# Kernel tuning notes

Hardware: AMD Instinct MI355X
Metric: run time of the kernel (lower is better)

## Reference

```python
import jax, jax.numpy as jnp
import numpy as np

TOP_K = 2000
NUM_DETS = 1000
BASE_LAYER_RANGE = (24.0, 48.0, 24.0, 48.0)  # (min_y, max_y, min_x, max_x) from db.configs


def _topk(heat, K):
    # heat: [B, C, H, W] -> topk over flattened C*H*W (CornerNet-style)
    B, C, H, W = heat.shape
    scores, inds = jax.lax.top_k(heat.reshape(B, -1), K)
    clses = inds // (H * W)
    sp_inds = inds % (H * W)            # spatial index into H*W
    ys = (sp_inds // W).astype(heat.dtype)
    xs = (sp_inds % W).astype(heat.dtype)
    return scores, sp_inds, clses, ys, xs


def _transpose_and_gather(feat, ind):
    # feat: [B, C, H, W], ind: [B, K] spatial indices -> [B, K, C]
    B, C, H, W = feat.shape
    feat = feat.transpose(0, 2, 3, 1).reshape(B, H * W, C)
    return feat[jnp.arange(B)[:, None], ind]


def _gather_feat(feat, ind):
    # feat: [B, N, C], ind: [B, K] -> [B, K, C]
    B = feat.shape[0]
    return feat[jnp.arange(B)[:, None], ind]


def _decode_layer(heat, tl_regr, br_regr, H0, W0, layer_idx):
    B, C, H, W = heat.shape
    dt = heat.dtype
    height_scale = 8.0 * H0 / H
    width_scale = 8.0 * W0 / W
    K = min(TOP_K, H * W)
    scores, inds, clses, ys, xs = _topk(heat, K)
    ys = ys.reshape(B, K, 1)
    xs = xs.reshape(B, K, 1)
    tlr = _transpose_and_gather(tl_regr, inds).reshape(B, K, 1, 2)
    brr = _transpose_and_gather(br_regr, inds).reshape(B, K, 1, 2)
    min_y, max_y, min_x, max_x = [v / 8.0 / 2.0 for v in BASE_LAYER_RANGE]
    tl_xs = xs - ((max_x - min_x) * tlr[..., 0] + (max_x + min_x) / 2.0)
    tl_ys = ys - ((max_y - min_y) * tlr[..., 1] + (max_y + min_y) / 2.0)
    br_xs = xs + ((max_x - min_x) * brr[..., 0] + (max_x + min_x) / 2.0)
    br_ys = ys + ((max_y - min_y) * brr[..., 1] + (max_y + min_y) / 2.0)
    bboxes = jnp.stack((tl_xs, tl_ys, br_xs, br_ys), axis=3)  # [B, K, 1, 4]
    sc = scores.reshape(B, K, 1)
    invalid = (br_xs < tl_xs) | (br_ys < tl_ys)
    sc = jnp.where(invalid, jnp.asarray(-1.0, dt), sc)
    sc = sc.reshape(B, -1)
    nd = min(NUM_DETS, sc.shape[1])
    sc, top = jax.lax.top_k(sc, nd)
    sc = sc[:, :, None]
    bboxes = _gather_feat(bboxes.reshape(B, -1, 4), top)
    bboxes = bboxes * jnp.asarray([width_scale, height_scale, width_scale, height_scale], dt)
    # layer_detections: zeros [B, nd, 7]; [:,:,:5] = cat([scores, bboxes]); then row 6 set to i
    det = jnp.concatenate([sc, bboxes, jnp.zeros((B, nd, 2), dt)], axis=2)
    det = det.at[:, 6, :].set(jnp.asarray(float(layer_idx), dt))  # faithful to `[:, 6] = i`
    return det


def setup_inputs() -> dict:
    key = jax.random.key(0)
    ks = jax.random.split(key, 9)
    B, C = 16, 80
    sizes = [(128, 128), (64, 64), (32, 32)]
    inp = {}
    for i, (H, W) in enumerate(sizes):
        inp[f"heat{i}"] = jax.random.uniform(ks[3 * i], (B, C, H, W), dtype=jnp.float32)
        inp[f"tl{i}"] = jax.random.normal(ks[3 * i + 1], (B, 2, H, W), dtype=jnp.float32)
        inp[f"br{i}"] = jax.random.normal(ks[3 * i + 2], (B, 2, H, W), dtype=jnp.float32)
    return inp


def reference(heat0, heat1, heat2, tl0, tl1, tl2, br0, br1, br2):
    heats = [heat0, heat1, heat2]
    tls = [tl0, tl1, tl2]
    brs = [br0, br1, br2]
    _, _, H0, W0 = heats[0].shape
    dets = [_decode_layer(heats[i], tls[i], brs[i], H0, W0, i) for i in range(3)]
    detections = jnp.concatenate(dets, axis=1)  # [B, sum_nd, 7]
    nd = min(NUM_DETS, detections.shape[1])
    _, top = jax.lax.top_k(detections[:, :, 0], nd)
    return _gather_feat(detections, top)
```

## Files before the change

### kernel.cpp

```cpp
#include <hip/hip_runtime.h>


#define NB 1024
#define CHUNK 32768

__device__ __forceinline__ unsigned int ord_f32(float f) {
    unsigned int b = __float_as_uint(f);
    return (b & 0x80000000u) ? ~b : (b | 0x80000000u);
}
__device__ __forceinline__ float unord_f32(unsigned int o) {
    unsigned int b = (o & 0x80000000u) ? (o & 0x7fffffffu) : ~o;
    return __uint_as_float(b);
}
__device__ __forceinline__ int bucket_of(float f) {
    int bi = (int)(f * (float)NB);
    bi = bi < 0 ? 0 : (bi > NB - 1 ? NB - 1 : bi);
    return bi;
}

__device__ __forceinline__ int layer_N(int l)   { return (l == 0) ? 1310720 : (l == 1) ? 327680 : 81920; }
__device__ __forceinline__ int nchunks(int l)   { return (l == 0) ? 40 : (l == 1) ? 10 : 3; }
__device__ __forceinline__ int chunk_base(int l){ return (l == 0) ? 0 : (l == 1) ? 640 : 800; }
__device__ __forceinline__ float TL_of(int l)   { return (l == 0) ? 0.998046875f : (l == 1) ? 0.9921875f : 0.98125f; }
__device__ __forceinline__ int seg_cap(int l)   { return (l == 0) ? 256 : (l == 1) ? 768 : 1024; }
__device__ __forceinline__ int loose_base(int l){ return (l == 0) ? 0 : (l == 1) ? 163840 : 286720; }

__global__ __launch_bounds__(256) void collect_kernel(
    const float* __restrict__ h0, const float* __restrict__ h1, const float* __restrict__ h2,
    int* __restrict__ pbc, unsigned long long* __restrict__ loose)
{
    int l = blockIdx.z, b = blockIdx.y, chunk = blockIdx.x;
    int nc = nchunks(l);
    if (chunk >= nc) return;
    int N = layer_N(l);
    int elems = min(CHUNK, N - chunk * CHUNK);
    const float* heat = (l == 0) ? h0 : (l == 1) ? h1 : h2;
    float TL = TL_of(l);

    __shared__ int lc;
    __shared__ unsigned long long lbuf[1024];
    if (threadIdx.x == 0) lc = 0;
    __syncthreads();

    const float4* p = (const float4*)(heat + (size_t)b * N + (size_t)chunk * CHUNK);
    int base = chunk * CHUNK;
    int n4 = elems >> 2;
    for (int i = threadIdx.x; i < n4; i += 256) {
        float4 v = p[i];
        float vs[4] = {v.x, v.y, v.z, v.w};
#pragma unroll
        for (int cc = 0; cc < 4; cc++) {
            if (vs[cc] >= TL) {
                int pos = atomicAdd(&lc, 1);
                if (pos < 1024) {
                    unsigned int idx = (unsigned int)(base + 4 * i + cc);
                    lbuf[pos] = ((unsigned long long)ord_f32(vs[cc]) << 32) | (unsigned int)(~idx);
                }
            }
        }
    }
    __syncthreads();
    int pidx = chunk_base(l) + b * nc + chunk;
    if (threadIdx.x == 0) pbc[pidx] = lc;
    int cap = seg_cap(l);
    int n = min(lc, cap);
    unsigned long long* seg = loose + loose_base(l) + (size_t)(b * nc + chunk) * cap;
    for (int i = threadIdx.x; i < n; i += 256) seg[i] = lbuf[i];
}


__device__ __forceinline__ unsigned long long shfl_xor_u64(unsigned long long a, int j) {
    unsigned int lo = (unsigned int)a, hi = (unsigned int)(a >> 32);
    lo = (unsigned int)__shfl_xor((int)lo, j, 64);
    hi = (unsigned int)__shfl_xor((int)hi, j, 64);
    return ((unsigned long long)hi << 32) | lo;
}

template<int K, int J>
struct P16 {
    static __device__ __forceinline__ void run(unsigned long long (&v)[16], int base, int lane) {
        constexpr int JR = J >> 6;
#pragma unroll
        for (int r = 0; r < 16; r++) {
            if ((r & JR) == 0) {
                int i = base | (r << 6) | lane;
                unsigned long long a = v[r], bb = v[r | JR];
                bool sw = ((i & K) == 0) ? (a < bb) : (a > bb);
                if (sw) { v[r] = bb; v[r | JR] = a; }
            }
        }
        P16<K, (J >> 1)>::run(v, base, lane);
    }
};

template<int K>
struct P16<K, 32> {
    static __device__ __forceinline__ void run(unsigned long long (&v)[16], int base, int lane) {
#pragma unroll
        for (int js = 32; js >= 1; js >>= 1) {
            if (K > js) {
#pragma unroll
                for (int r = 0; r < 16; r++) {
                    unsigned long long a = v[r];
                    unsigned long long w = shfl_xor_u64(a, js);
                    int i = base | (r << 6) | lane;
                    bool upper = (lane & js) != 0;
                    bool keep_max = (((i & K) == 0) != upper);
                    bool agw = a > w;
                    v[r] = (keep_max == agw) ? a : w;
                }
            }
        }
    }
};

template<int K>
struct S16 {
    static __device__ __forceinline__ void run(unsigned long long (&v)[16], int base, int lane) {
        P16<K, (K > 64 ? (K >> 1) : 32)>::run(v, base, lane);
        S16<(K << 1)>::run(v, base, lane);
    }
};
template<>
struct S16<2048> {
    static __device__ __forceinline__ void run(unsigned long long (&)[16], int, int) {}
};

template<int K, int J>
__device__ __forceinline__ void lds_exchange16(unsigned long long (&v)[16],
                                               unsigned long long* lds, int base, int lane) {
    __syncthreads();
#pragma unroll
    for (int r = 0; r < 16; r++) lds[base | (r << 6) | lane] = v[r];
    __syncthreads();
#pragma unroll
    for (int r = 0; r < 16; r++) {
        int i = base | (r << 6) | lane;
        unsigned long long w = lds[i ^ J];
        bool upper = (i & J) != 0;
        bool keep_max = (((i & K) == 0) != upper);
        bool agw = v[r] > w;
        v[r] = (keep_max == agw) ? v[r] : w;
    }
}

__global__ __launch_bounds__(256) void sort_kernel(
    const float* __restrict__ h0, const float* __restrict__ h1, const float* __restrict__ h2,
    const int* __restrict__ pbc, const unsigned long long* __restrict__ loose,
    unsigned long long* __restrict__ cand)
{
    int bl = blockIdx.x;
    int l = bl >> 4, b = bl & 15;
    int K = (l == 2) ? 1024 : 2000;
    int nc = nchunks(l);
    int cap = seg_cap(l);
    int tid = threadIdx.x;
    int lane = tid & 63;
    int base = (tid >> 6) << 10;

    __shared__ unsigned long long lds[4096];
    __shared__ int offs[41];
    __shared__ int s_bad, s_tot;

    if (tid == 0) {
        int o = 0, bad = 0;
        const int* pb = pbc + chunk_base(l) + b * nc;
        for (int c = 0; c < nc; c++) {
            int raw = pb[c];
            if (raw > cap) bad = 1;
            offs[c] = o;
            o += min(raw, cap);
        }
        offs[nc] = o;
        if (o < K || o > 4096) bad = 1;
        s_bad = bad;
        s_tot = o;
    }
    __syncthreads();

    if (!s_bad) {
        const unsigned long long* lb = loose + loose_base(l) + (size_t)b * nc * cap;
        for (int c = 0; c < nc; c++) {
            int o = offs[c], n_c = offs[c + 1] - o;
            const unsigned long long* sg = lb + (size_t)c * cap;
            for (int i = tid; i < n_c; i += 256) lds[o + i] = sg[i];
        }
        for (int i = s_tot + tid; i < 4096; i += 256) lds[i] = 0ull;
    } else {
        __shared__ int lh[NB];
        __shared__ int st, lc2;
        for (int i = tid; i < NB; i += 256) lh[i] = 0;
        if (tid == 0) lc2 = 0;
        __syncthreads();
        int N = layer_N(l);
        const float* hp = ((l == 0) ? h0 : (l == 1) ? h1 : h2) + (size_t)b * N;
        for (int i = tid; i < N; i += 256) atomicAdd(&lh[bucket_of(hp[i])], 1);
        __syncthreads();
        if (tid == 0) {
            int acc = 0, bidx;
            for (bidx = NB - 1; bidx > 0; bidx--) {
                acc += lh[bidx];
                if (acc >= K) break;
            }
            st = bidx;
        }
        __syncthreads();
        int t = st;
        for (int i = tid; i < N; i += 256) {
            float x = hp[i];
            if (bucket_of(x) >= t) {
                int pos = atomicAdd(&lc2, 1);
                if (pos < 4096)
                    lds[pos] = ((unsigned long long)ord_f32(x) << 32) | (unsigned int)(~(unsigned int)i);
            }
        }
        __syncthreads();
        for (int i = min(lc2, 4096) + tid; i < 4096; i += 256) lds[i] = 0ull;
    }
    __syncthreads();

    unsigned long long v[16];
#pragma unroll
    for (int r = 0; r < 16; r++) v[r] = lds[base | (r << 6) | lane];

    S16<2>::run(v, base, lane);

    lds_exchange16<2048, 1024>(v, lds, base, lane);
    P16<2048, 512>::run(v, base, lane);

    lds_exchange16<4096, 2048>(v, lds, base, lane);
    lds_exchange16<4096, 1024>(v, lds, base, lane);
    P16<4096, 512>::run(v, base, lane);

    unsigned long long* cd = cand + (size_t)bl * 4096;
#pragma unroll
    for (int r = 0; r < 16; r++) cd[base | (r << 6) | lane] = v[r];
}

__global__ __launch_bounds__(1024) void build_kernel(
    const float* __restrict__ t0, const float* __restrict__ t1, const float* __restrict__ t2,
    const float* __restrict__ r0, const float* __restrict__ r1, const float* __restrict__ r2,
    const unsigned long long* __restrict__ cand, float* __restrict__ det)
{
    int l = blockIdx.x >> 4;
    int b = blockIdx.x & 15;
    int bl = l * 16 + b;
    int HW = (l == 0) ? 16384 : (l == 1) ? 4096 : 1024;
    int W  = (l == 0) ? 128 : (l == 1) ? 64 : 32;
    int K  = (l == 2) ? 1024 : 2000;
    float scale = (l == 0) ? 8.f : (l == 1) ? 16.f : 32.f;
    const float* tlp = (l == 0) ? t0 : (l == 1) ? t1 : t2;
    const float* brp = (l == 0) ? r0 : (l == 1) ? r1 : r2;

    const unsigned long long* srt = cand + (size_t)bl * 4096;

    __shared__ int wsum[16];
    int tid = threadIdx.x;
    int lane = tid & 63, wid = tid >> 6;

    float s_[2], bx_[2][4];
    int f_[2];
#pragma unroll
    for (int q = 0; q < 2; q++) {
        int k = 2 * tid + q;
        f_[q] = 0;
        if (k < K) {
            unsigned long long kk = srt[k];
            unsigned int idx = ~(unsigned int)kk;
            float score = unord_f32((unsigned int)(kk >> 32));
            int sp = (int)(idx % (unsigned)HW);
            float xs = (float)(sp % W), ys = (float)(sp / W);
            float tv0 = tlp[((size_t)b * 2 + 0) * HW + sp];
            float tv1 = tlp[((size_t)b * 2 + 1) * HW + sp];
            float bv0 = brp[((size_t)b * 2 + 0) * HW + sp];
            float bv1 = brp[((size_t)b * 2 + 1) * HW + sp];
            float tlx = __fsub_rn(xs, __fadd_rn(__fmul_rn(1.5f, tv0), 2.25f));
            float tly = __fsub_rn(ys, __fadd_rn(__fmul_rn(1.5f, tv1), 2.25f));
            float brx = __fadd_rn(xs, __fadd_rn(__fmul_rn(1.5f, bv0), 2.25f));
            float bry = __fadd_rn(ys, __fadd_rn(__fmul_rn(1.5f, bv1), 2.25f));
            bool invalid = (brx < tlx) || (bry < tly);
            f_[q] = invalid ? 0 : 1;
            s_[q] = invalid ? -1.0f : score;
            bx_[q][0] = __fmul_rn(tlx, scale);
            bx_[q][1] = __fmul_rn(tly, scale);
            bx_[q][2] = __fmul_rn(brx, scale);
            bx_[q][3] = __fmul_rn(bry, scale);
        }
    }
    int mysum = f_[0] + f_[1];

    int x = mysum;
#pragma unroll
    for (int off = 1; off < 64; off <<= 1) {
        int y = __shfl_up(x, off, 64);
        if (lane >= off) x += y;
    }
    if (lane == 63) wsum[wid] = x;
    __syncthreads();
    if (wid == 0 && lane < 16) {
        int s = wsum[lane];
#pragma unroll
        for (int off = 1; off < 16; off <<= 1) {
            int y = __shfl_up(s, off, 64);
            if (lane >= off) s += y;
        }
        wsum[lane] = s;
    }
    __syncthreads();
    int wave_off = (wid > 0) ? wsum[wid - 1] : 0;
    int V = wsum[15];
    int base_excl = (x + wave_off) - mysum;

    float* dbase = det + ((size_t)b * 3000 + (size_t)l * 1000) * 7;
#pragma unroll
    for (int q = 0; q < 2; q++) {
        int k = 2 * tid + q;
        if (k < K) {
            int pos = base_excl + (q == 1 ? f_[0] : 0);
            int rank = f_[q] ? pos : V + (k - pos);
            if (rank < 1000 && rank != 6) {
                float* drow = dbase + (size_t)rank * 7;
                drow[0] = s_[q];
                drow[1] = bx_[q][0];
                drow[2] = bx_[q][1];
                drow[3] = bx_[q][2];
                drow[4] = bx_[q][3];
                drow[5] = 0.f;
                drow[6] = 0.f;
            }
        }
    }
    if (tid == 0) {
        float lv = (float)l;
        float* drow = dbase + 6 * 7;
#pragma unroll
        for (int j = 0; j < 7; j++) drow[j] = lv;
    }
}

__device__ __forceinline__ bool key_gt(float sa, int ga, float sb, int gb) {
    return (sa > sb) || (sa == sb && ga < gb);
}

__global__ __launch_bounds__(1024) void final_kernel(const float* __restrict__ det,
                                                     float* __restrict__ out)
{
    int b = blockIdx.x;
    __shared__ float sc[3000];
    int tid = threadIdx.x;
    const float* dbase = det + (size_t)b * 3000 * 7;
    for (int i = tid; i < 3000; i += 1024) sc[i] = dbase[(size_t)i * 7];
    __syncthreads();

    for (int e = tid; e < 3000; e += 1024) {
        float se = sc[e];
        int ge = e;
        int rank = 0;
#pragma unroll
        for (int lp = 0; lp < 3; lp++) {
            int lo = 0, hiB = 999;
            while (lo < hiB) {
                int mid = (lo + hiB) >> 1;
                int p = mid + (mid >= 6 ? 1 : 0);
                int g = lp * 1000 + p;
                if (key_gt(sc[g], g, se, ge)) lo = mid + 1; else hiB = mid;
            }
            rank += lo;
        }
#pragma unroll
        for (int ls = 0; ls < 3; ls++) {
            int g = ls * 1000 + 6;
            if (g != e && key_gt((float)ls, g, se, ge)) rank++;
        }
        if (rank < 1000) {
            const float* src = dbase + (size_t)e * 7;
            float* dst = out + ((size_t)b * 1000 + rank) * 7;
#pragma unroll
            for (int j = 0; j < 7; j++) dst[j] = src[j];
        }
    }
}

extern "C" void kernel_launch(void* const* d_in, const int* in_sizes, int n_in,
                              void* d_out, int out_size, void* d_ws, size_t ws_size,
                              hipStream_t stream)
{
    (void)in_sizes; (void)n_in; (void)out_size; (void)ws_size;
    const float* h0 = (const float*)d_in[0];
    const float* t0 = (const float*)d_in[1];
    const float* r0 = (const float*)d_in[2];
    const float* h1 = (const float*)d_in[3];
    const float* t1 = (const float*)d_in[4];
    const float* r1 = (const float*)d_in[5];
    const float* h2 = (const float*)d_in[6];
    const float* t2 = (const float*)d_in[7];
    const float* r2 = (const float*)d_in[8];
    float* out = (float*)d_out;

    char* ws = (char*)d_ws;
    int* pbc  = (int*)ws;
    unsigned long long* loose = (unsigned long long*)(ws + 3392);
    unsigned long long* cand  = (unsigned long long*)(ws + 2690368);
    float* det = (float*)(ws + 4263232);

    collect_kernel<<<dim3(40, 16, 3), 256, 0, stream>>>(h0, h1, h2, pbc, loose);
    sort_kernel<<<48, 256, 0, stream>>>(h0, h1, h2, pbc, loose, cand);
    build_kernel<<<48, 1024, 0, stream>>>(t0, t1, t2, r0, r1, r2, cand, det);
    final_kernel<<<16, 1024, 0, stream>>>(det, out);
}
```

Measured before the change: 249.6 us.

## Replace full bitonic sort with per-wave sorts and rank-based merge

The sort kernel now runs 512 threads, and each wave bitonic-sorts 512 keys in registers instead of 1024. The final cross-wave bitonic stages with LDS exchanges are replaced by a merge-by-rank: each key binary-searches the other seven sorted lists and scatters to its global position. Padding becomes unique small values so ranks do not collide. The change trades barrier-heavy exchange stages for many dependent LDS binary-search reads.

```diff
diff --git a/kernel.cpp b/kernel.cpp
--- a/kernel.cpp
+++ b/kernel.cpp
@@ -68,7 +68,6 @@
     for (int i = threadIdx.x; i < n; i += 256) seg[i] = lbuf[i];
 }
 
-
 __device__ __forceinline__ unsigned long long shfl_xor_u64(unsigned long long a, int j) {
     unsigned int lo = (unsigned int)a, hi = (unsigned int)(a >> 32);
     lo = (unsigned int)__shfl_xor((int)lo, j, 64);
@@ -77,33 +76,33 @@
 }
 
 template<int K, int J>
-struct P16 {
-    static __device__ __forceinline__ void run(unsigned long long (&v)[16], int base, int lane) {
+struct PhaseH {
+    static __device__ __forceinline__ void run(unsigned long long (&v)[8], int lane) {
         constexpr int JR = J >> 6;
 #pragma unroll
-        for (int r = 0; r < 16; r++) {
+        for (int r = 0; r < 8; r++) {
             if ((r & JR) == 0) {
-                int i = base | (r << 6) | lane;
+                int i = (r << 6) | lane;
                 unsigned long long a = v[r], bb = v[r | JR];
                 bool sw = ((i & K) == 0) ? (a < bb) : (a > bb);
                 if (sw) { v[r] = bb; v[r | JR] = a; }
             }
         }
-        P16<K, (J >> 1)>::run(v, base, lane);
+        PhaseH<K, (J >> 1)>::run(v, lane);
     }
 };
 
 template<int K>
-struct P16<K, 32> {
-    static __device__ __forceinline__ void run(unsigned long long (&v)[16], int base, int lane) {
+struct PhaseH<K, 32> {
+    static __device__ __forceinline__ void run(unsigned long long (&v)[8], int lane) {
 #pragma unroll
         for (int js = 32; js >= 1; js >>= 1) {
             if (K > js) {
 #pragma unroll
-                for (int r = 0; r < 16; r++) {
+                for (int r = 0; r < 8; r++) {
                     unsigned long long a = v[r];
                     unsigned long long w = shfl_xor_u64(a, js);
-                    int i = base | (r << 6) | lane;
+                    int i = (r << 6) | lane;
                     bool upper = (lane & js) != 0;
                     bool keep_max = (((i & K) == 0) != upper);
                     bool agw = a > w;
@@ -115,36 +114,18 @@
 };
 
 template<int K>
-struct S16 {
-    static __device__ __forceinline__ void run(unsigned long long (&v)[16], int base, int lane) {
-        P16<K, (K > 64 ? (K >> 1) : 32)>::run(v, base, lane);
-        S16<(K << 1)>::run(v, base, lane);
+struct StageH {
+    static __device__ __forceinline__ void run(unsigned long long (&v)[8], int lane) {
+        PhaseH<K, (K > 64 ? (K >> 1) : 32)>::run(v, lane);
+        StageH<(K << 1)>::run(v, lane);
     }
 };
 template<>
-struct S16<2048> {
-    static __device__ __forceinline__ void run(unsigned long long (&)[16], int, int) {}
+struct StageH<1024> {
+    static __device__ __forceinline__ void run(unsigned long long (&)[8], int) {}
 };
 
-template<int K, int J>
-__device__ __forceinline__ void lds_exchange16(unsigned long long (&v)[16],
-                                               unsigned long long* lds, int base, int lane) {
-    __syncthreads();
-#pragma unroll
-    for (int r = 0; r < 16; r++) lds[base | (r << 6) | lane] = v[r];
-    __syncthreads();
-#pragma unroll
-    for (int r = 0; r < 16; r++) {
-        int i = base | (r << 6) | lane;
-        unsigned long long w = lds[i ^ J];
-        bool upper = (i & J) != 0;
-        bool keep_max = (((i & K) == 0) != upper);
-        bool agw = v[r] > w;
-        v[r] = (keep_max == agw) ? v[r] : w;
-    }
-}
-
-__global__ __launch_bounds__(256) void sort_kernel(
+__global__ __launch_bounds__(512) void sort_kernel(
     const float* __restrict__ h0, const float* __restrict__ h1, const float* __restrict__ h2,
     const int* __restrict__ pbc, const unsigned long long* __restrict__ loose,
     unsigned long long* __restrict__ cand)
@@ -156,9 +137,10 @@
     int cap = seg_cap(l);
     int tid = threadIdx.x;
     int lane = tid & 63;
-    int base = (tid >> 6) << 10;
-
-    __shared__ unsigned long long lds[4096];
+    int wid = tid >> 6;
+
+    __shared__ unsigned long long A[4096];
+    __shared__ unsigned long long Bq[4096];
     __shared__ int offs[41];
     __shared__ int s_bad, s_tot;
 
@@ -183,18 +165,18 @@
         for (int c = 0; c < nc; c++) {
             int o = offs[c], n_c = offs[c + 1] - o;
             const unsigned long long* sg = lb + (size_t)c * cap;
-            for (int i = tid; i < n_c; i += 256) lds[o + i] = sg[i];
-        }
-        for (int i = s_tot + tid; i < 4096; i += 256) lds[i] = 0ull;
+            for (int i = tid; i < n_c; i += 512) A[o + i] = sg[i];
+        }
+        for (int i = s_tot + tid; i < 4096; i += 512) A[i] = (unsigned long long)i;
     } else {
         __shared__ int lh[NB];
         __shared__ int st, lc2;
-        for (int i = tid; i < NB; i += 256) lh[i] = 0;
+        for (int i = tid; i < NB; i += 512) lh[i] = 0;
         if (tid == 0) lc2 = 0;
         __syncthreads();
         int N = layer_N(l);
         const float* hp = ((l == 0) ? h0 : (l == 1) ? h1 : h2) + (size_t)b * N;
-        for (int i = tid; i < N; i += 256) atomicAdd(&lh[bucket_of(hp[i])], 1);
+        for (int i = tid; i < N; i += 512) atomicAdd(&lh[bucket_of(hp[i])], 1);
         __syncthreads();
         if (tid == 0) {
             int acc = 0, bidx;
@@ -206,35 +188,50 @@
         }
         __syncthreads();
         int t = st;
-        for (int i = tid; i < N; i += 256) {
+        for (int i = tid; i < N; i += 512) {
             float x = hp[i];
             if (bucket_of(x) >= t) {
                 int pos = atomicAdd(&lc2, 1);
                 if (pos < 4096)
-                    lds[pos] = ((unsigned long long)ord_f32(x) << 32) | (unsigned int)(~(unsigned int)i);
+                    A[pos] = ((unsigned long long)ord_f32(x) << 32) | (unsigned int)(~(unsigned int)i);
             }
         }
         __syncthreads();
-        for (int i = min(lc2, 4096) + tid; i < 4096; i += 256) lds[i] = 0ull;
-    }
-    __syncthreads();
-
-    unsigned long long v[16];
-#pragma unroll
-    for (int r = 0; r < 16; r++) v[r] = lds[base | (r << 6) | lane];
-
-    S16<2>::run(v, base, lane);
-
-    lds_exchange16<2048, 1024>(v, lds, base, lane);
-    P16<2048, 512>::run(v, base, lane);
-
-    lds_exchange16<4096, 2048>(v, lds, base, lane);
-    lds_exchange16<4096, 1024>(v, lds, base, lane);
-    P16<4096, 512>::run(v, base, lane);
+        for (int i = min(lc2, 4096) + tid; i < 4096; i += 512) A[i] = (unsigned long long)i;
+    }
+    __syncthreads();
+
+    int base = wid << 9;
+    unsigned long long v[8];
+#pragma unroll
+    for (int r = 0; r < 8; r++) v[r] = A[base | (r << 6) | lane];
+
+    StageH<2>::run(v, lane);
+
+#pragma unroll
+    for (int r = 0; r < 8; r++) A[base | (r << 6) | lane] = v[r];
+    __syncthreads();
+
+#pragma unroll
+    for (int r = 0; r < 8; r++) {
+        unsigned long long key = v[r];
+        int rank = (r << 6) | lane;
+        for (int w2 = 0; w2 < 8; w2++) {
+            if (w2 == wid) continue;
+            const unsigned long long* Lw = A + (w2 << 9);
+            int lo = 0, hi = 512;
+            while (lo < hi) {
+                int mid = (lo + hi) >> 1;
+                if (Lw[mid] > key) lo = mid + 1; else hi = mid;
+            }
+            rank += lo;
+        }
+        Bq[rank] = key;
+    }
+    __syncthreads();
 
     unsigned long long* cd = cand + (size_t)bl * 4096;
-#pragma unroll
-    for (int r = 0; r < 16; r++) cd[base | (r << 6) | lane] = v[r];
+    for (int i = tid; i < 4096; i += 512) cd[i] = Bq[i];
 }
 
 __global__ __launch_bounds__(1024) void build_kernel(
@@ -404,7 +401,7 @@
     float* det = (float*)(ws + 4263232);
 
     collect_kernel<<<dim3(40, 16, 3), 256, 0, stream>>>(h0, h1, h2, pbc, loose);
-    sort_kernel<<<48, 256, 0, stream>>>(h0, h1, h2, pbc, loose, cand);
+    sort_kernel<<<48, 512, 0, stream>>>(h0, h1, h2, pbc, loose, cand);
     build_kernel<<<48, 1024, 0, stream>>>(t0, t1, t2, r0, r1, r2, cand, det);
     final_kernel<<<16, 1024, 0, stream>>>(det, out);
 }
```

Result: slower. 267.6 us (+7.2%).
